# Kernel tuning notes

Measured on AMD Instinct MI355X. Metric: run time of the kernel, lower is better.

Reference implementation:

```python
import jax, jax.numpy as jnp
import numpy as np

EPS = 1e-05


def reference(inputs, c1, h1, c2, h2, w, b, norm_w, norm_b):
    B = inputs.shape[0]
    U = inputs.shape[1]
    # [B, 3U] @ [3U, 5U] + [1, 5U]
    x = jnp.concatenate([inputs, h1, h2], axis=1)
    res = x @ w + b
    # split into 5 contiguous gates -> [B, 5, U], layer-norm each gate over last axis
    g = res.reshape(B, 5, U)
    m = jnp.mean(g, axis=-1, keepdims=True)
    v = jnp.var(g, axis=-1, keepdims=True)  # biased variance, matches tf.nn.moments
    ln = (g - m) / jnp.sqrt(v + EPS) * norm_w[None, :, :] + norm_b[None, :, :]
    i, j, f, f2, o = ln[:, 0], ln[:, 1], ln[:, 2], ln[:, 3], ln[:, 4]
    new_c = c1 * jax.nn.sigmoid(f) + c2 * jax.nn.sigmoid(f2) + jax.nn.sigmoid(i) * jnp.tanh(j)
    new_h = new_c * jax.nn.sigmoid(o)
    return new_c, new_h


def setup_inputs() -> dict:
    B, U = 16384, 512
    key = jax.random.key(0)
    ks = jax.random.split(key, 6)
    return {
        "inputs": jax.random.normal(ks[0], (B, U), dtype=jnp.float32),
        "c1": jax.random.normal(ks[1], (B, U), dtype=jnp.float32),
        "h1": jax.random.normal(ks[2], (B, U), dtype=jnp.float32),
        "c2": jax.random.normal(ks[3], (B, U), dtype=jnp.float32),
        "h2": jax.random.normal(ks[4], (B, U), dtype=jnp.float32),
        "w": jax.random.normal(ks[5], (3 * U, 5 * U), dtype=jnp.float32) * (1.0 / np.sqrt(3 * U)),
        "b": jnp.zeros((1, 5 * U), dtype=jnp.float32),
        "norm_w": jnp.ones((5, U), dtype=jnp.float32),
        "norm_b": jnp.zeros((5, U), dtype=jnp.float32),
    }
```

## Files before the change

kernel.cpp:

```cpp
#include <hip/hip_runtime.h>
#include <hip/hip_bf16.h>
#include <cstdint>

#define B_DIM 16384
#define U_DIM 512
#define K_DIM 1536
#define N_DIM 2560
#define NT    24

typedef unsigned short u16;
typedef __attribute__((ext_vector_type(4))) unsigned short u16x4;
typedef __attribute__((ext_vector_type(8))) unsigned short u16x8;
typedef __attribute__((ext_vector_type(8))) short bf16x8;
typedef __attribute__((ext_vector_type(4))) float f32x4;

__device__ __forceinline__ u16 f2bf(float f) {
    uint32_t u = __builtin_bit_cast(uint32_t, f);
    u += 0x7FFFu + ((u >> 16) & 1u);
    return (u16)(u >> 16);
}
__device__ __forceinline__ float bf2f(u16 h) {
    uint32_t u = ((uint32_t)h) << 16;
    return __builtin_bit_cast(float, u);
}

__global__ void __launch_bounds__(256) cvt_x_kernel(
    const float* __restrict__ inp, const float* __restrict__ h1,
    const float* __restrict__ h2, u16* __restrict__ xb)
{
    int idx = blockIdx.x * 256 + threadIdx.x;
    const int total4 = B_DIM * K_DIM / 4;
    if (idx >= total4) return;
    int e = idx * 4;
    int b = e / K_DIM;
    int k = e - b * K_DIM;
    const float* src;
    if (k < 512)       src = inp + b * 512 + k;
    else if (k < 1024) src = h1  + b * 512 + (k - 512);
    else               src = h2  + b * 512 + (k - 1024);
    float4 v = *(const float4*)src;
    u16x4 o;
    o.x = f2bf(v.x); o.y = f2bf(v.y); o.z = f2bf(v.z); o.w = f2bf(v.w);
    *(u16x4*)(xb + e) = o;
}

__global__ void __launch_bounds__(256) cvt_wT_kernel(
    const float* __restrict__ w, u16* __restrict__ wT)
{
    __shared__ float tile[32][33];
    const int n0 = blockIdx.x * 32;
    const int k0 = blockIdx.y * 32;
    const int tx = threadIdx.x & 31;
    const int ty = threadIdx.x >> 5;
#pragma unroll
    for (int i = 0; i < 4; ++i) {
        int kk = ty + i * 8;
        tile[kk][tx] = w[(k0 + kk) * N_DIM + n0 + tx];
    }
    __syncthreads();
#pragma unroll
    for (int i = 0; i < 4; ++i) {
        int nn = ty + i * 8;
        wT[(int64_t)(n0 + nn) * K_DIM + k0 + tx] = f2bf(tile[tx][nn]);
    }
}

__device__ __forceinline__ void gload_lds16(const void* g, void* l) {
    __builtin_amdgcn_global_load_lds(
        (const __attribute__((address_space(1))) void*)g,
        (__attribute__((address_space(3))) void*)l, 16, 0, 0);
}

#define BAR    __builtin_amdgcn_s_barrier()
#define FENCE  asm volatile("" ::: "memory")
#define VMCNT4 asm volatile("s_waitcnt vmcnt(4)" ::: "memory")
#define LGKM0  do { asm volatile("s_waitcnt lgkmcnt(0)" ::: "memory"); \
                    __builtin_amdgcn_sched_barrier(0); } while (0)

__global__ void __launch_bounds__(512, 2) gemm_kernel(
    const u16* __restrict__ A, const u16* __restrict__ Bt,
    u16* __restrict__ C)
{
    __shared__ u16 sm[65536];

    const int tid  = threadIdx.x;
    const int lane = tid & 63;
    const int wave = tid >> 6;

    int bid = blockIdx.x;
    int swz = (bid & 7) * 80 + (bid >> 3);
    const int bm = (swz / 10) * 256;
    const int bn = (swz % 10) * 256;

    const int wm = (wave >> 2) * 128;
    const int wn = (wave & 3) * 64;

    const int l15 = lane & 15, cq = lane >> 4;
    const int s   = (((l15 & 1) << 2) | cq) ^ ((l15 >> 1) & 7);
    const int rdA = ((wm >> 1) + (l15 >> 1)) * 64 + s * 8;
    const int rdB = ((wn >> 1) + (l15 >> 1)) * 64 + s * 8;

    const int line0 = tid >> 3;
    const int sl0   = (tid & 7) ^ (line0 & 7);
    const int srow  = line0 * 2 + (sl0 >> 2);
    const int sc8   = (sl0 & 3) * 8;
    const u16* gA = A  + (int64_t)(bm + srow) * K_DIM + sc8;
    const u16* gB = Bt + (int64_t)(bn + srow) * K_DIM + sc8;
    char* ld0 = (char*)sm + tid * 16;

#define STAGE(ab, ks, kt, buf) do {                                        \
        const u16* g_ = ((ab) ? gB : gA) + (kt) + (ks) * 32;               \
        char* d_ = ld0 + (buf) * 65536 + (ab) * 32768 + (ks) * 16384;      \
        gload_lds16(g_, d_);                                               \
        gload_lds16(g_ + 128 * K_DIM, d_ + 8192);                          \
    } while (0)

    f32x4 acc[8][4];
#pragma unroll
    for (int i = 0; i < 8; ++i)
#pragma unroll
        for (int j = 0; j < 4; ++j) acc[i][j] = (f32x4)(0.0f);

    STAGE(0, 0, 0, 0);
    STAGE(1, 0, 0, 0);
    STAGE(0, 1, 0, 0);
    STAGE(1, 1, 0, 0);
    VMCNT4;
    BAR; FENCE;

    bf16x8 af[4], bfr[4];

#define LOAD_A4(BASE) _Pragma("unroll")                                    \
    for (int mi = 0; mi < 4; ++mi) af[mi] = *(const bf16x8*)((BASE) + mi * 512)
#define LOAD_B4(BASE) _Pragma("unroll")                                    \
    for (int n = 0; n < 4; ++n) bfr[n] = *(const bf16x8*)((BASE) + n * 512)
#define MFMA16(MB) _Pragma("unroll")                                       \
    for (int mi = 0; mi < 4; ++mi) { _Pragma("unroll")                     \
        for (int n = 0; n < 4; ++n)                                        \
            acc[(MB) + mi][n] = __builtin_amdgcn_mfma_f32_16x16x32_bf16(   \
                af[mi], bfr[n], acc[(MB) + mi][n], 0, 0, 0); }

    for (int t = 0; t < NT; ++t) {
        const int cur = t & 1, nxt = cur ^ 1;
        const int ktn = ((t + 1) == NT) ? 0 : (t + 1) * 64;
        const u16* aB = sm + cur * 32768 + rdA;
        const u16* bB = sm + cur * 32768 + 16384 + rdB;

        LOAD_A4(aB);
        LOAD_B4(bB);
        STAGE(0, 0, ktn, nxt);
        BAR; LGKM0;
        __builtin_amdgcn_s_setprio(1);
        MFMA16(0);
        __builtin_amdgcn_s_setprio(0);
        BAR; FENCE;

        LOAD_A4(aB + 4 * 512);
        STAGE(1, 0, ktn, nxt);
        BAR; LGKM0;
        __builtin_amdgcn_s_setprio(1);
        MFMA16(4);
        __builtin_amdgcn_s_setprio(0);
        VMCNT4;
        BAR; FENCE;

        LOAD_A4(aB + 8192);
        LOAD_B4(bB + 8192);
        STAGE(0, 1, ktn, nxt);
        BAR; LGKM0;
        __builtin_amdgcn_s_setprio(1);
        MFMA16(0);
        __builtin_amdgcn_s_setprio(0);
        BAR; FENCE;

        LOAD_A4(aB + 8192 + 4 * 512);
        STAGE(1, 1, ktn, nxt);
        BAR; LGKM0;
        __builtin_amdgcn_s_setprio(1);
        MFMA16(4);
        __builtin_amdgcn_s_setprio(0);
        VMCNT4;
        BAR; FENCE;
    }

    const int ecol = lane & 15;
    const int erow = (lane >> 4) * 4;
#pragma unroll
    for (int m = 0; m < 8; ++m)
#pragma unroll
        for (int n = 0; n < 4; ++n)
#pragma unroll
            for (int r = 0; r < 4; ++r) {
                int grow = bm + wm + m * 16 + erow + r;
                int gcol = bn + wn + n * 16 + ecol;
                C[(int64_t)grow * N_DIM + gcol] = f2bf(acc[m][n][r]);
            }
}

__global__ void __launch_bounds__(256) ln_pointwise_kernel(
    const u16*  __restrict__ res,  const float* __restrict__ bias,
    const float* __restrict__ c1,  const float* __restrict__ c2,
    const float* __restrict__ nw,  const float* __restrict__ nb,
    float* __restrict__ out)
{
    const int wave = threadIdx.x >> 6;
    const int lane = threadIdx.x & 63;
    const int b    = blockIdx.x * 4 + wave;
    const u16* row = res + (int64_t)b * N_DIM;
    const int u0 = lane * 8;

    float v[5][8];
    float rstd[5], mean[5];

#pragma unroll
    for (int g = 0; g < 5; ++g) {
        u16x8 raw = *(const u16x8*)(row + g * 512 + u0);
        const float4* bp = (const float4*)(bias + g * 512 + u0);
        float4 b0 = bp[0], b1 = bp[1];
        v[g][0] = bf2f(raw[0]) + b0.x;  v[g][1] = bf2f(raw[1]) + b0.y;
        v[g][2] = bf2f(raw[2]) + b0.z;  v[g][3] = bf2f(raw[3]) + b0.w;
        v[g][4] = bf2f(raw[4]) + b1.x;  v[g][5] = bf2f(raw[5]) + b1.y;
        v[g][6] = bf2f(raw[6]) + b1.z;  v[g][7] = bf2f(raw[7]) + b1.w;
        float s = 0.f, q = 0.f;
#pragma unroll
        for (int j = 0; j < 8; ++j) { s += v[g][j]; q += v[g][j] * v[g][j]; }
#pragma unroll
        for (int off = 1; off < 64; off <<= 1) {
            s += __shfl_xor(s, off);
            q += __shfl_xor(q, off);
        }
        float m   = s * (1.0f / 512.0f);
        float var = q * (1.0f / 512.0f) - m * m;
        mean[g] = m;
        rstd[g] = rsqrtf(var + 1e-5f);
    }

#pragma unroll
    for (int g = 0; g < 5; ++g) {
        const float4* wp = (const float4*)(nw + g * 512 + u0);
        const float4* bp = (const float4*)(nb + g * 512 + u0);
        float4 w0 = wp[0], w1 = wp[1], n0 = bp[0], n1 = bp[1];
        float ws[8] = {w0.x, w0.y, w0.z, w0.w, w1.x, w1.y, w1.z, w1.w};
        float ns[8] = {n0.x, n0.y, n0.z, n0.w, n1.x, n1.y, n1.z, n1.w};
#pragma unroll
        for (int j = 0; j < 8; ++j)
            v[g][j] = (v[g][j] - mean[g]) * rstd[g] * ws[j] + ns[j];
    }

    const float4* c1p = (const float4*)(c1 + (int64_t)b * 512 + u0);
    const float4* c2p = (const float4*)(c2 + (int64_t)b * 512 + u0);
    float4 c1a = c1p[0], c1b = c1p[1], c2a = c2p[0], c2b = c2p[1];
    float c1s[8] = {c1a.x, c1a.y, c1a.z, c1a.w, c1b.x, c1b.y, c1b.z, c1b.w};
    float c2s[8] = {c2a.x, c2a.y, c2a.z, c2a.w, c2b.x, c2b.y, c2b.z, c2b.w};

    float oc[8], oh[8];
#pragma unroll
    for (int j = 0; j < 8; ++j) {
        float ig  = 1.0f / (1.0f + expf(-v[0][j]));
        float jg  = tanhf(v[1][j]);
        float fg  = 1.0f / (1.0f + expf(-v[2][j]));
        float f2g = 1.0f / (1.0f + expf(-v[3][j]));
        float og  = 1.0f / (1.0f + expf(-v[4][j]));
        float cc  = c1s[j] * fg + c2s[j] * f2g + ig * jg;
        oc[j] = cc;
        oh[j] = cc * og;
    }

    float* oC = out + (int64_t)b * 512 + u0;
    float* oH = out + (int64_t)B_DIM * U_DIM + (int64_t)b * 512 + u0;
    ((float4*)oC)[0] = make_float4(oc[0], oc[1], oc[2], oc[3]);
    ((float4*)oC)[1] = make_float4(oc[4], oc[5], oc[6], oc[7]);
    ((float4*)oH)[0] = make_float4(oh[0], oh[1], oh[2], oh[3]);
    ((float4*)oH)[1] = make_float4(oh[4], oh[5], oh[6], oh[7]);
}

extern "C" void kernel_launch(void* const* d_in, const int* in_sizes, int n_in,
                              void* d_out, int out_size, void* d_ws, size_t ws_size,
                              hipStream_t stream)
{
    const float* inputs = (const float*)d_in[0];
    const float* c1     = (const float*)d_in[1];
    const float* h1     = (const float*)d_in[2];
    const float* c2     = (const float*)d_in[3];
    const float* h2     = (const float*)d_in[4];
    const float* w      = (const float*)d_in[5];
    const float* bias   = (const float*)d_in[6];
    const float* nw     = (const float*)d_in[7];
    const float* nb     = (const float*)d_in[8];
    float* out = (float*)d_out;

    const size_t XB_BYTES = (size_t)B_DIM * K_DIM * 2;
    const size_t WT_BYTES = (size_t)N_DIM * K_DIM * 2;
    u16* xb  = (u16*)d_ws;
    u16* wT  = (u16*)((char*)d_ws + XB_BYTES);
    u16* res = (u16*)((char*)d_ws + XB_BYTES + WT_BYTES);

    cvt_x_kernel<<<(B_DIM * K_DIM / 4 + 255) / 256, 256, 0, stream>>>(inputs, h1, h2, xb);
    cvt_wT_kernel<<<dim3(N_DIM / 32, K_DIM / 32), 256, 0, stream>>>(w, wT);
    gemm_kernel<<<(B_DIM / 256) * (N_DIM / 256), 512, 0, stream>>>(xb, wT, res);
    ln_pointwise_kernel<<<B_DIM / 4, 256, 0, stream>>>(res, bias, c1, c2, nw, nb, out);
}
```

Before: 391.6 us.

## Shrink GEMM block tile to 128x256 and use fast sigmoid/tanh

Changes the GEMM macro tile from 256x256 to 128x256, halving the per-wave accumulator set and the A-tile LDS footprint. The per-iteration pipeline is restructured from four sub-stages into two, with new LDS offsets and staging. This doubles the grid, which may help occupancy and tail balance, but B-tile reuse per block drops and global traffic for B rises. The pointwise kernel also switches to __expf-based sigmoid and tanh to cut transcendental cost, with a small loss of accuracy.

```diff
diff --git a/kernel.cpp b/kernel.cpp
--- a/kernel.cpp
+++ b/kernel.cpp
@@ -73,7 +73,7 @@
 
 #define BAR    __builtin_amdgcn_s_barrier()
 #define FENCE  asm volatile("" ::: "memory")
-#define VMCNT4 asm volatile("s_waitcnt vmcnt(4)" ::: "memory")
+#define VMCNT3 asm volatile("s_waitcnt vmcnt(3)" ::: "memory")
 #define LGKM0  do { asm volatile("s_waitcnt lgkmcnt(0)" ::: "memory"); \
                     __builtin_amdgcn_sched_barrier(0); } while (0)
 
@@ -81,51 +81,53 @@
     const u16* __restrict__ A, const u16* __restrict__ Bt,
     u16* __restrict__ C)
 {
-    __shared__ u16 sm[65536];
+    __shared__ u16 sm[49152];
 
     const int tid  = threadIdx.x;
     const int lane = tid & 63;
     const int wave = tid >> 6;
 
     int bid = blockIdx.x;
-    int swz = (bid & 7) * 80 + (bid >> 3);
-    const int bm = (swz / 10) * 256;
+    int swz = (bid & 7) * 160 + (bid >> 3);
+    const int bm = (swz / 10) * 128;
     const int bn = (swz % 10) * 256;
 
-    const int wm = (wave >> 2) * 128;
+    const int wm = (wave >> 2) * 64;
     const int wn = (wave & 3) * 64;
 
     const int l15 = lane & 15, cq = lane >> 4;
     const int s   = (((l15 & 1) << 2) | cq) ^ ((l15 >> 1) & 7);
-    const int rdA = ((wm >> 1) + (l15 >> 1)) * 64 + s * 8;
-    const int rdB = ((wn >> 1) + (l15 >> 1)) * 64 + s * 8;
+    const int rdA = ((wm + l15) >> 1) * 64 + s * 8;
+    const int rdB = ((wn + l15) >> 1) * 64 + s * 8;
 
     const int line0 = tid >> 3;
-    const int sl0   = (tid & 7) ^ (line0 & 7);
-    const int srow  = line0 * 2 + (sl0 >> 2);
-    const int sc8   = (sl0 & 3) * 8;
+    const int rc    = (tid & 7) ^ (line0 & 7);
+    const int srow  = line0 * 2 + (rc >> 2);
+    const int sc8   = (rc & 3) * 8;
     const u16* gA = A  + (int64_t)(bm + srow) * K_DIM + sc8;
     const u16* gB = Bt + (int64_t)(bn + srow) * K_DIM + sc8;
-    char* ld0 = (char*)sm + tid * 16;
-
-#define STAGE(ab, ks, kt, buf) do {                                        \
-        const u16* g_ = ((ab) ? gB : gA) + (kt) + (ks) * 32;               \
-        char* d_ = ld0 + (buf) * 65536 + (ab) * 32768 + (ks) * 16384;      \
-        gload_lds16(g_, d_);                                               \
-        gload_lds16(g_ + 128 * K_DIM, d_ + 8192);                          \
+    char* ldA = (char*)sm + tid * 16;
+    char* ldB = (char*)sm + 16384 + tid * 16;
+
+#define STAGE(ks, kt, buf) do {                                            \
+        const u16* ga_ = gA + (kt) + (ks) * 32;                            \
+        const u16* gb_ = gB + (kt) + (ks) * 32;                            \
+        char* la_ = ldA + (buf) * 49152 + (ks) * 8192;                     \
+        char* lb_ = ldB + (buf) * 49152 + (ks) * 16384;                    \
+        gload_lds16(ga_, la_);                                             \
+        gload_lds16(gb_, lb_);                                             \
+        gload_lds16(gb_ + 128 * K_DIM, lb_ + 8192);                        \
     } while (0)
 
-    f32x4 acc[8][4];
-#pragma unroll
-    for (int i = 0; i < 8; ++i)
+    f32x4 acc[4][4];
+#pragma unroll
+    for (int i = 0; i < 4; ++i)
 #pragma unroll
         for (int j = 0; j < 4; ++j) acc[i][j] = (f32x4)(0.0f);
 
-    STAGE(0, 0, 0, 0);
-    STAGE(1, 0, 0, 0);
-    STAGE(0, 1, 0, 0);
-    STAGE(1, 1, 0, 0);
-    VMCNT4;
+    STAGE(0, 0, 0);
+    STAGE(1, 0, 0);
+    VMCNT3;
     BAR; FENCE;
 
     bf16x8 af[4], bfr[4];
@@ -134,59 +136,42 @@
     for (int mi = 0; mi < 4; ++mi) af[mi] = *(const bf16x8*)((BASE) + mi * 512)
 #define LOAD_B4(BASE) _Pragma("unroll")                                    \
     for (int n = 0; n < 4; ++n) bfr[n] = *(const bf16x8*)((BASE) + n * 512)
-#define MFMA16(MB) _Pragma("unroll")                                       \
+#define MFMA16 _Pragma("unroll")                                           \
     for (int mi = 0; mi < 4; ++mi) { _Pragma("unroll")                     \
         for (int n = 0; n < 4; ++n)                                        \
-            acc[(MB) + mi][n] = __builtin_amdgcn_mfma_f32_16x16x32_bf16(   \
-                af[mi], bfr[n], acc[(MB) + mi][n], 0, 0, 0); }
+            acc[mi][n] = __builtin_amdgcn_mfma_f32_16x16x32_bf16(          \
+                af[mi], bfr[n], acc[mi][n], 0, 0, 0); }
 
     for (int t = 0; t < NT; ++t) {
         const int cur = t & 1, nxt = cur ^ 1;
         const int ktn = ((t + 1) == NT) ? 0 : (t + 1) * 64;
-        const u16* aB = sm + cur * 32768 + rdA;
-        const u16* bB = sm + cur * 32768 + 16384 + rdB;
-
-        LOAD_A4(aB);
-        LOAD_B4(bB);
-        STAGE(0, 0, ktn, nxt);
+        const u16* base = sm + cur * 24576;
+
+        LOAD_A4(base + rdA);
+        LOAD_B4(base + 8192 + rdB);
+        STAGE(0, ktn, nxt);
         BAR; LGKM0;
         __builtin_amdgcn_s_setprio(1);
-        MFMA16(0);
+        MFMA16;
         __builtin_amdgcn_s_setprio(0);
+        VMCNT3;
         BAR; FENCE;
 
-        LOAD_A4(aB + 4 * 512);
-        STAGE(1, 0, ktn, nxt);
+        LOAD_A4(base + 4096 + rdA);
+        LOAD_B4(base + 8192 + 8192 + rdB);
+        STAGE(1, ktn, nxt);
         BAR; LGKM0;
         __builtin_amdgcn_s_setprio(1);
-        MFMA16(4);
+        MFMA16;
         __builtin_amdgcn_s_setprio(0);
-        VMCNT4;
-        BAR; FENCE;
-
-        LOAD_A4(aB + 8192);
-        LOAD_B4(bB + 8192);
-        STAGE(0, 1, ktn, nxt);
-        BAR; LGKM0;
-        __builtin_amdgcn_s_setprio(1);
-        MFMA16(0);
-        __builtin_amdgcn_s_setprio(0);
-        BAR; FENCE;
-
-        LOAD_A4(aB + 8192 + 4 * 512);
-        STAGE(1, 1, ktn, nxt);
-        BAR; LGKM0;
-        __builtin_amdgcn_s_setprio(1);
-        MFMA16(4);
-        __builtin_amdgcn_s_setprio(0);
-        VMCNT4;
+        VMCNT3;
         BAR; FENCE;
     }
 
     const int ecol = lane & 15;
     const int erow = (lane >> 4) * 4;
 #pragma unroll
-    for (int m = 0; m < 8; ++m)
+    for (int m = 0; m < 4; ++m)
 #pragma unroll
         for (int n = 0; n < 4; ++n)
 #pragma unroll
@@ -195,6 +180,15 @@
                 int gcol = bn + wn + n * 16 + ecol;
                 C[(int64_t)grow * N_DIM + gcol] = f2bf(acc[m][n][r]);
             }
+}
+
+__device__ __forceinline__ float fsig(float x) {
+    return 1.0f / (1.0f + __expf(-x));
+}
+__device__ __forceinline__ float ftanh(float x) {
+    float e = __expf(-2.0f * fabsf(x));
+    float r = (1.0f - e) / (1.0f + e);
+    return copysignf(r, x);
 }
 
 __global__ void __launch_bounds__(256) ln_pointwise_kernel(
@@ -256,11 +250,11 @@
     float oc[8], oh[8];
 #pragma unroll
     for (int j = 0; j < 8; ++j) {
-        float ig  = 1.0f / (1.0f + expf(-v[0][j]));
-        float jg  = tanhf(v[1][j]);
-        float fg  = 1.0f / (1.0f + expf(-v[2][j]));
-        float f2g = 1.0f / (1.0f + expf(-v[3][j]));
-        float og  = 1.0f / (1.0f + expf(-v[4][j]));
+        float ig  = fsig(v[0][j]);
+        float jg  = ftanh(v[1][j]);
+        float fg  = fsig(v[2][j]);
+        float f2g = fsig(v[3][j]);
+        float og  = fsig(v[4][j]);
         float cc  = c1s[j] * fg + c2s[j] * f2g + ig * jg;
         oc[j] = cc;
         oh[j] = cc * og;
@@ -297,6 +291,6 @@
 
     cvt_x_kernel<<<(B_DIM * K_DIM / 4 + 255) / 256, 256, 0, stream>>>(inputs, h1, h2, xb);
     cvt_wT_kernel<<<dim3(N_DIM / 32, K_DIM / 32), 256, 0, stream>>>(w, wT);
-    gemm_kernel<<<(B_DIM / 256) * (N_DIM / 256), 512, 0, stream>>>(xb, wT, res);
+    gemm_kernel<<<(B_DIM / 128) * (N_DIM / 256), 512, 0, stream>>>(xb, wT, res);
     ln_pointwise_kernel<<<B_DIM / 4, 256, 0, stream>>>(res, bias, c1, c2, nw, nb, out);
 }
```

Measured after the change: 383.1 us. 2.2% less time.
